# Kernel tuning notes

Hardware: AMD Instinct MI355X
Metric: run time of the kernel (lower is better)

## Reference

```python
import jax, jax.numpy as jnp
import numpy as np

D_MODEL, NHEAD = 1024, 16
DK = D_MODEL // NHEAD


def setup_inputs() -> dict:
    key = jax.random.key(0)
    ks = jax.random.split(key, 10)
    B, T = 2, 2048
    s = 1.0 / np.sqrt(D_MODEL)
    inp = {
        "x": jax.random.normal(ks[0], (B, T, D_MODEL), dtype=jnp.float32),
        "attn_bias": jax.random.normal(ks[1], (1, NHEAD, T, T), dtype=jnp.float32),
        "Wq": jax.random.normal(ks[2], (D_MODEL, D_MODEL), dtype=jnp.float32) * s,
        "bq": jnp.zeros((D_MODEL,), dtype=jnp.float32),
        "Wk": jax.random.normal(ks[3], (D_MODEL, D_MODEL), dtype=jnp.float32) * s,
        "bk": jnp.zeros((D_MODEL,), dtype=jnp.float32),
        "Wv": jax.random.normal(ks[4], (D_MODEL, D_MODEL), dtype=jnp.float32) * s,
        "bv": jnp.zeros((D_MODEL,), dtype=jnp.float32),
        "Wo": jax.random.normal(ks[5], (D_MODEL, D_MODEL), dtype=jnp.float32) * s,
        "bo": jnp.zeros((D_MODEL,), dtype=jnp.float32),
    }
    return inp


def reference(x, attn_bias, Wq, bq, Wk, bk, Wv, bv, Wo, bo):
    B, T, D = x.shape
    H, dk = NHEAD, DK
    # torch Linear: y = x @ W.T + b
    q = (x @ Wq.T + bq).reshape(B, T, H, dk).transpose(0, 2, 1, 3)  # [B,H,T,dk]
    k = (x @ Wk.T + bk).reshape(B, T, H, dk).transpose(0, 2, 1, 3)
    v = (x @ Wv.T + bv).reshape(B, T, H, dk).transpose(0, 2, 1, 3)
    scores = jnp.einsum("bhqd,bhkd->bhqk", q, k) / jnp.sqrt(jnp.float32(dk))
    scores = scores + attn_bias  # broadcast over batch
    attn = jax.nn.softmax(scores, axis=-1)  # dropout p=0.0 -> identity
    out = jnp.einsum("bhqk,bhkd->bhqd", attn, v)
    out = out.transpose(0, 2, 1, 3).reshape(B, T, D)
    return out @ Wo.T + bo
```

## Files before the change

kernel.cpp:

```cpp
#include <hip/hip_runtime.h>

typedef unsigned short u16;
typedef unsigned int u32;
using short8 = __attribute__((ext_vector_type(8))) short;
using f32x4  = __attribute__((ext_vector_type(4))) float;

#define D_MODEL 1024
#define NHEAD 16
#define DKV 64
#define TSEQ 2048
#define BATCH 2
#define L2E 1.44269504f
#define CSHIFT 12.0f

#define GLOAD16(gp, lp)                                                      \
    __builtin_amdgcn_global_load_lds(                                        \
        (const __attribute__((address_space(1))) u32*)(gp),                  \
        (__attribute__((address_space(3))) u32*)(lp), 16, 0, 0)

__device__ __forceinline__ u16 f2bf(float f) {
    union { float f; u32 i; } c; c.f = f;
    u32 x = c.i;
    return (u16)((x + 0x7FFFu + ((x >> 16) & 1u)) >> 16);
}
__device__ __forceinline__ u16 f2bf_fast(float f) {
    union { float f; u32 i; } c; c.f = f;
    return (u16)((c.i + 0x8000u) >> 16);
}

__global__ __launch_bounds__(256) void prep_cvt(
    const float* __restrict__ x,  const float* __restrict__ Wq,
    const float* __restrict__ Wk, const float* __restrict__ Wv,
    const float* __restrict__ Wo, u16* __restrict__ dst)
{
    size_t e = ((size_t)blockIdx.x * 256 + threadIdx.x) * 8;
    const float* src; size_t off;
    if (e < 4194304u)      { src = x;  off = e; }
    else if (e < 5242880u) { src = Wq; off = e - 4194304u; }
    else if (e < 6291456u) { src = Wk; off = e - 5242880u; }
    else if (e < 7340032u) { src = Wv; off = e - 6291456u; }
    else                   { src = Wo; off = e - 7340032u; }
    float4 a = *(const float4*)(src + off);
    float4 b = *(const float4*)(src + off + 4);
    short8 v;
    v[0] = (short)f2bf(a.x); v[1] = (short)f2bf(a.y);
    v[2] = (short)f2bf(a.z); v[3] = (short)f2bf(a.w);
    v[4] = (short)f2bf(b.x); v[5] = (short)f2bf(b.y);
    v[6] = (short)f2bf(b.z); v[7] = (short)f2bf(b.w);
    *(short8*)(dst + e) = v;
}

__global__ __launch_bounds__(256) void qkv_gemm(
    const u16* __restrict__ xbf, const u16* __restrict__ wbf,
    const float* __restrict__ bq, const float* __restrict__ bk,
    const float* __restrict__ bv, u16* __restrict__ qkv)
{
    __shared__ __align__(16) u16 Alds[128 * 64];
    __shared__ __align__(16) u16 Blds[128 * 64];

    const int fid = blockIdx.x;
    const int xcd = fid & 7, ii = fid >> 3;
    const int z = ii >> 5, r2 = ii & 31;
    const int nb = r2 & 7, mb = xcd * 4 + (r2 >> 3);
    const int n0 = nb * 128, m0 = mb * 128;
    const u16* W = wbf + (size_t)z * 1048576;
    const float* bias = (z == 0) ? bq : (z == 1) ? bk : bv;
    u16* out = qkv + (size_t)z * 4194304;

    const int t = threadIdx.x;
    const int wave = t >> 6, lane = t & 63, l15 = lane & 15, quad = lane >> 4;
    const int wm = (wave >> 1) * 64, wn = (wave & 1) * 64;

    f32x4 acc[4][4];
#pragma unroll
    for (int i = 0; i < 4; ++i)
#pragma unroll
        for (int j = 0; j < 4; ++j)
#pragma unroll
            for (int r = 0; r < 4; ++r) acc[i][j][r] = 0.f;

    const int rs = t >> 3, cs = (t & 7) * 8;
    const u16* ga = xbf + (size_t)(m0 + rs) * 1024 + cs;
    const u16* gb = W   + (size_t)(n0 + rs) * 1024 + cs;
    u16* la = &Alds[rs * 64 + cs];
    u16* lb = &Blds[rs * 64 + cs];

    for (int kt = 0; kt < 16; ++kt) {
        const int k0 = kt * 64;
#pragma unroll
        for (int c = 0; c < 4; ++c) {
            GLOAD16(ga + (size_t)(c * 32) * 1024 + k0, la + c * 32 * 64);
            GLOAD16(gb + (size_t)(c * 32) * 1024 + k0, lb + c * 32 * 64);
        }
        __syncthreads();
#pragma unroll
        for (int ki = 0; ki < 2; ++ki) {
            short8 af[4], bfr[4];
#pragma unroll
            for (int i = 0; i < 4; ++i)
                af[i] = *(const short8*)&Alds[(wm + i * 16 + l15) * 64 + ki * 32 + quad * 8];
#pragma unroll
            for (int j = 0; j < 4; ++j)
                bfr[j] = *(const short8*)&Blds[(wn + j * 16 + l15) * 64 + ki * 32 + quad * 8];
#pragma unroll
            for (int i = 0; i < 4; ++i)
#pragma unroll
                for (int j = 0; j < 4; ++j)
                    acc[i][j] = __builtin_amdgcn_mfma_f32_16x16x32_bf16(af[i], bfr[j], acc[i][j], 0, 0, 0);
        }
        __syncthreads();
    }

#pragma unroll
    for (int j = 0; j < 4; ++j) {
        int n = n0 + wn + j * 16 + l15;
        float bb = bias[n];
        int h = n >> 6, d = n & 63;
#pragma unroll
        for (int i = 0; i < 4; ++i)
#pragma unroll
            for (int r = 0; r < 4; ++r) {
                int m = m0 + wm + i * 16 + quad * 4 + r;
                int bidx = m >> 11, tt = m & 2047;
                out[(((size_t)(bidx * NHEAD + h)) * TSEQ + tt) * DKV + d] =
                    f2bf(acc[i][j][r] + bb);
            }
    }
}

__global__ __launch_bounds__(256) void attn_kernel(
    const u16* __restrict__ qws, const u16* __restrict__ kws, const u16* __restrict__ vws,
    const float* __restrict__ bias, u16* __restrict__ ows)
{
    __shared__ __align__(16) u16 Klds[64 * 72];
    __shared__ __align__(16) u16 Vt[2][64 * 72];
    __shared__ __align__(16) u16 Plds[64 * 72];

    const int fid = blockIdx.x;
    const int xcd = fid & 7, ii = fid >> 3;
    const int bh = xcd * 4 + (ii >> 5);
    const int qt = ii & 31;
    const int h = bh & 15;
    const int q0 = qt * 64;
    const int t = threadIdx.x;
    const int wave = t >> 6, lane = t & 63, l15 = lane & 15, quad = lane >> 4;
    const size_t bhoff = (size_t)bh * TSEQ * DKV;

    short8 qa0, qa1;
    {
        const u16* qp = qws + bhoff + (size_t)(q0 + wave * 16 + l15) * DKV;
        qa0 = *(const short8*)(qp + quad * 8);
        qa1 = *(const short8*)(qp + 32 + quad * 8);
    }

    float l_run[4] = {0.f, 0.f, 0.f, 0.f};
    f32x4 o_acc[4];
#pragma unroll
    for (int db = 0; db < 4; ++db)
#pragma unroll
        for (int r = 0; r < 4; ++r) o_acc[db][r] = 0.f;

    const float* bias_h = bias + ((size_t)h * TSEQ + q0) * TSEQ;
    const int a8 = t & 7, c8 = a8 * 8, rp = t >> 3;
    const int rbase = wave * 16 + quad * 4;

    for (int kt = 0; kt < TSEQ / 64; ++kt) {
        const int kc0 = kt * 64;
        u16* vtb = &Vt[kt & 1][0];

        float bz[16];
#pragma unroll
        for (int cb = 0; cb < 4; ++cb)
#pragma unroll
            for (int r = 0; r < 4; ++r)
                bz[cb * 4 + r] =
                    bias_h[(size_t)(rbase + r) * TSEQ + kc0 + cb * 16 + l15];

        {
            const u16* kp = kws + bhoff + (size_t)(kc0 + rp) * DKV + c8;
            short8 k0 = *(const short8*)kp;
            short8 k1 = *(const short8*)(kp + 32 * DKV);
            *(short8*)&Klds[rp * 72 + c8] = k0;
            *(short8*)&Klds[(rp + 32) * 72 + c8] = k1;
        }
        {
            const u16* vp = vws + bhoff + (size_t)(kc0 + 2 * rp) * DKV + c8;
            short8 v0 = *(const short8*)vp;
            short8 v1 = *(const short8*)(vp + DKV);
            int bk = rp >> 2;
            int kcl = (2 * rp) & 7;
#pragma unroll
            for (int j = 0; j < 8; ++j) {
                int d = c8 + j;
                u32 val = ((u32)(u16)v0[j]) | (((u32)(u16)v1[j]) << 16);
                *(u32*)&vtb[d * 72 + ((bk ^ a8) * 8) + kcl] = val;
            }
        }
        __syncthreads();

        f32x4 s[4];
#pragma unroll
        for (int cb = 0; cb < 4; ++cb)
#pragma unroll
            for (int r = 0; r < 4; ++r) s[cb][r] = 0.f;
#pragma unroll
        for (int cb = 0; cb < 4; ++cb) {
            const u16* kr = &Klds[(cb * 16 + l15) * 72 + quad * 8];
            short8 kb0 = *(const short8*)kr;
            short8 kb1 = *(const short8*)(kr + 32);
            s[cb] = __builtin_amdgcn_mfma_f32_16x16x32_bf16(qa0, kb0, s[cb], 0, 0, 0);
            s[cb] = __builtin_amdgcn_mfma_f32_16x16x32_bf16(qa1, kb1, s[cb], 0, 0, 0);
        }

#pragma unroll
        for (int cb = 0; cb < 4; ++cb)
#pragma unroll
            for (int r = 0; r < 4; ++r) {
                float arg = fmaf(s[cb][r], 0.125f * L2E,
                                 fmaf(bz[cb * 4 + r], L2E, -CSHIFT * L2E));
                float p = exp2f(fminf(arg, 43.f));
                l_run[r] += p;
                Plds[(rbase + r) * 72 + cb * 16 + l15] = f2bf_fast(p);
            }
        __syncthreads();

        {
            const u16* pr = &Plds[(wave * 16 + l15) * 72 + quad * 8];
            short8 pa0 = *(const short8*)pr;
            short8 pa1 = *(const short8*)(pr + 32);
#pragma unroll
            for (int db = 0; db < 4; ++db) {
                int d = db * 16 + l15;
                int sw = (d >> 3) & 7;
                const u16* vr = &vtb[d * 72];
                short8 vb0 = *(const short8*)(vr + ((quad ^ sw) * 8));
                short8 vb1 = *(const short8*)(vr + (((4 + quad) ^ sw) * 8));
                o_acc[db] = __builtin_amdgcn_mfma_f32_16x16x32_bf16(pa0, vb0, o_acc[db], 0, 0, 0);
                o_acc[db] = __builtin_amdgcn_mfma_f32_16x16x32_bf16(pa1, vb1, o_acc[db], 0, 0, 0);
            }
        }
    }

#pragma unroll
    for (int r = 0; r < 4; ++r) {
        float v = l_run[r];
        v += __shfl_xor(v, 1);
        v += __shfl_xor(v, 2);
        v += __shfl_xor(v, 4);
        v += __shfl_xor(v, 8);
        l_run[r] = v;
    }
#pragma unroll
    for (int r = 0; r < 4; ++r) {
        float inv = 1.f / l_run[r];
        int row = q0 + rbase + r;
#pragma unroll
        for (int db = 0; db < 4; ++db)
            ows[bhoff + (size_t)row * DKV + db * 16 + l15] = f2bf(o_acc[db][r] * inv);
    }
}

__global__ __launch_bounds__(256) void out_gemm(
    const u16* __restrict__ ows, const u16* __restrict__ wobf,
    const float* __restrict__ bo, float* __restrict__ out)
{
    __shared__ __align__(16) u16 Alds[128 * 64];
    __shared__ __align__(16) u16 Blds[128 * 64];

    const int fid = blockIdx.x;
    const int xcd = fid & 7, ii = fid >> 3;
    const int nb = ii & 7, mb = xcd * 4 + (ii >> 3);
    const int n0 = nb * 128, m0 = mb * 128;

    const int t = threadIdx.x;
    const int wave = t >> 6, lane = t & 63, l15 = lane & 15, quad = lane >> 4;
    const int wm = (wave >> 1) * 64, wn = (wave & 1) * 64;

    f32x4 acc[4][4];
#pragma unroll
    for (int i = 0; i < 4; ++i)
#pragma unroll
        for (int j = 0; j < 4; ++j)
#pragma unroll
            for (int r = 0; r < 4; ++r) acc[i][j][r] = 0.f;

    const int rs = t >> 3, cs = (t & 7) * 8;
    const int bidx = m0 >> 11, tt0 = m0 & 2047;
    const u16* gaBase = ows + (((size_t)(bidx * NHEAD)) * TSEQ + tt0 + rs) * DKV + cs;
    const u16* gb = wobf + (size_t)(n0 + rs) * 1024 + cs;
    u16* la = &Alds[rs * 64 + cs];
    u16* lb = &Blds[rs * 64 + cs];

    for (int kt = 0; kt < 16; ++kt) {
        const int k0 = kt * 64;
#pragma unroll
        for (int c = 0; c < 4; ++c) {
            GLOAD16(gaBase + ((size_t)kt * TSEQ + c * 32) * DKV, la + c * 32 * 64);
            GLOAD16(gb + (size_t)(c * 32) * 1024 + k0,           lb + c * 32 * 64);
        }
        __syncthreads();
#pragma unroll
        for (int ki = 0; ki < 2; ++ki) {
            short8 af[4], bfr[4];
#pragma unroll
            for (int i = 0; i < 4; ++i)
                af[i] = *(const short8*)&Alds[(wm + i * 16 + l15) * 64 + ki * 32 + quad * 8];
#pragma unroll
            for (int j = 0; j < 4; ++j)
                bfr[j] = *(const short8*)&Blds[(wn + j * 16 + l15) * 64 + ki * 32 + quad * 8];
#pragma unroll
            for (int i = 0; i < 4; ++i)
#pragma unroll
                for (int j = 0; j < 4; ++j)
                    acc[i][j] = __builtin_amdgcn_mfma_f32_16x16x32_bf16(af[i], bfr[j], acc[i][j], 0, 0, 0);
        }
        __syncthreads();
    }

#pragma unroll
    for (int j = 0; j < 4; ++j) {
        int n = n0 + wn + j * 16 + l15;
        float bb = bo[n];
#pragma unroll
        for (int i = 0; i < 4; ++i)
#pragma unroll
            for (int r = 0; r < 4; ++r) {
                int m = m0 + wm + i * 16 + quad * 4 + r;
                out[(size_t)m * 1024 + n] = acc[i][j][r] + bb;
            }
    }
}

extern "C" void kernel_launch(void* const* d_in, const int* in_sizes, int n_in,
                              void* d_out, int out_size, void* d_ws, size_t ws_size,
                              hipStream_t stream)
{
    const float* x  = (const float*)d_in[0];
    const float* ab = (const float*)d_in[1];
    const float* Wq = (const float*)d_in[2];
    const float* bq = (const float*)d_in[3];
    const float* Wk = (const float*)d_in[4];
    const float* bk = (const float*)d_in[5];
    const float* Wv = (const float*)d_in[6];
    const float* bv = (const float*)d_in[7];
    const float* Wo = (const float*)d_in[8];
    const float* bo = (const float*)d_in[9];
    float* out = (float*)d_out;

    u16* wsu = (u16*)d_ws;
    const size_t WBF = 4194304;
    const size_t QKV = 8388608;
    const size_t OWS = 20971520;
    const size_t QSZ = 4194304;

    prep_cvt<<<4096, 256, 0, stream>>>(x, Wq, Wk, Wv, Wo, wsu);
    qkv_gemm<<<768, 256, 0, stream>>>(wsu, wsu + WBF, bq, bk, bv, wsu + QKV);
    attn_kernel<<<1024, 256, 0, stream>>>(wsu + QKV, wsu + QKV + QSZ,
                                          wsu + QKV + 2 * QSZ, ab, wsu + OWS);
    out_gemm<<<256, 256, 0, stream>>>(wsu + OWS, wsu + WBF + 3 * 1048576, bo, out);
}
```

Before: 513.8 us.

## Process both batches of a head in one block to share bias reads

```diff
diff --git a/kernel.cpp b/kernel.cpp
--- a/kernel.cpp
+++ b/kernel.cpp
@@ -128,22 +128,25 @@
     }
 }
 
-__global__ __launch_bounds__(256) void attn_kernel(
+__global__ __launch_bounds__(512, 4) void attn_kernel(
     const u16* __restrict__ qws, const u16* __restrict__ kws, const u16* __restrict__ vws,
     const float* __restrict__ bias, u16* __restrict__ ows)
 {
-    __shared__ __align__(16) u16 Klds[64 * 72];
-    __shared__ __align__(16) u16 Vt[2][64 * 72];
-    __shared__ __align__(16) u16 Plds[64 * 72];
+    __shared__ __align__(16) u16 Klds[2][64 * 72];
+    __shared__ __align__(16) u16 Vt[2][2][64 * 72];
+    __shared__ __align__(16) u16 Plds[2][64 * 72];
 
     const int fid = blockIdx.x;
     const int xcd = fid & 7, ii = fid >> 3;
-    const int bh = xcd * 4 + (ii >> 5);
+    const int h = xcd * 2 + (ii >> 5);
     const int qt = ii & 31;
-    const int h = bh & 15;
     const int q0 = qt * 64;
+
     const int t = threadIdx.x;
-    const int wave = t >> 6, lane = t & 63, l15 = lane & 15, quad = lane >> 4;
+    const int bg = t >> 8;
+    const int tl = t & 255;
+    const int wave = tl >> 6, lane = tl & 63, l15 = lane & 15, quad = lane >> 4;
+    const int bh = bg * NHEAD + h;
     const size_t bhoff = (size_t)bh * TSEQ * DKV;
 
     short8 qa0, qa1;
@@ -161,12 +164,12 @@
         for (int r = 0; r < 4; ++r) o_acc[db][r] = 0.f;
 
     const float* bias_h = bias + ((size_t)h * TSEQ + q0) * TSEQ;
-    const int a8 = t & 7, c8 = a8 * 8, rp = t >> 3;
+    const int a8 = tl & 7, c8 = a8 * 8, rp = tl >> 3;
     const int rbase = wave * 16 + quad * 4;
 
     for (int kt = 0; kt < TSEQ / 64; ++kt) {
         const int kc0 = kt * 64;
-        u16* vtb = &Vt[kt & 1][0];
+        u16* vtb = &Vt[bg][kt & 1][0];
 
         float bz[16];
 #pragma unroll
@@ -180,8 +183,8 @@
             const u16* kp = kws + bhoff + (size_t)(kc0 + rp) * DKV + c8;
             short8 k0 = *(const short8*)kp;
             short8 k1 = *(const short8*)(kp + 32 * DKV);
-            *(short8*)&Klds[rp * 72 + c8] = k0;
-            *(short8*)&Klds[(rp + 32) * 72 + c8] = k1;
+            *(short8*)&Klds[bg][rp * 72 + c8] = k0;
+            *(short8*)&Klds[bg][(rp + 32) * 72 + c8] = k1;
         }
         {
             const u16* vp = vws + bhoff + (size_t)(kc0 + 2 * rp) * DKV + c8;
@@ -205,7 +208,7 @@
             for (int r = 0; r < 4; ++r) s[cb][r] = 0.f;
 #pragma unroll
         for (int cb = 0; cb < 4; ++cb) {
-            const u16* kr = &Klds[(cb * 16 + l15) * 72 + quad * 8];
+            const u16* kr = &Klds[bg][(cb * 16 + l15) * 72 + quad * 8];
             short8 kb0 = *(const short8*)kr;
             short8 kb1 = *(const short8*)(kr + 32);
             s[cb] = __builtin_amdgcn_mfma_f32_16x16x32_bf16(qa0, kb0, s[cb], 0, 0, 0);
@@ -220,12 +223,12 @@
                                  fmaf(bz[cb * 4 + r], L2E, -CSHIFT * L2E));
                 float p = exp2f(fminf(arg, 43.f));
                 l_run[r] += p;
-                Plds[(rbase + r) * 72 + cb * 16 + l15] = f2bf_fast(p);
+                Plds[bg][(rbase + r) * 72 + cb * 16 + l15] = f2bf_fast(p);
             }
         __syncthreads();
 
         {
-            const u16* pr = &Plds[(wave * 16 + l15) * 72 + quad * 8];
+            const u16* pr = &Plds[bg][(wave * 16 + l15) * 72 + quad * 8];
             short8 pa0 = *(const short8*)pr;
             short8 pa1 = *(const short8*)(pr + 32);
 #pragma unroll
@@ -355,7 +358,7 @@
 
     prep_cvt<<<4096, 256, 0, stream>>>(x, Wq, Wk, Wv, Wo, wsu);
     qkv_gemm<<<768, 256, 0, stream>>>(wsu, wsu + WBF, bq, bk, bv, wsu + QKV);
-    attn_kernel<<<1024, 256, 0, stream>>>(wsu + QKV, wsu + QKV + QSZ,
-                                          wsu + QKV + 2 * QSZ, ab, wsu + OWS);
+    attn_kernel<<<512, 512, 0, stream>>>(wsu + QKV, wsu + QKV + QSZ,
+                                         wsu + QKV + 2 * QSZ, ab, wsu + OWS);
     out_gemm<<<256, 256, 0, stream>>>(wsu + OWS, wsu + WBF + 3 * 1048576, bo, out);
 }
```

After: 507.1 us. No clear change (-1.3%).
